# Performance work log

Hardware: AMD Instinct MI355X
Metric: run time of the kernel (lower is better)

The kernel has to match this reference:

```python
import jax, jax.numpy as jnp
import numpy as np

HP, WP = 8, 8          # stoken_size
N_ITER = 2             # refinement iterations
EPS = 1e-12


def unfold3(x):
    """3x3 neighborhood extraction (identity-kernel conv2d, padding=1).
    x: (B, C, hh, ww) -> (B, C, 9, hh, ww); channel k = shift (k//3-1, k%3-1)."""
    B, C, hh, ww = x.shape
    xp = jnp.pad(x, ((0, 0), (0, 0), (1, 1), (1, 1)))
    return jnp.stack([xp[:, :, i:i + hh, j:j + ww]
                      for i in range(3) for j in range(3)], axis=2)


def fold3(x):
    """Transpose of unfold3 (identity-kernel conv_transpose2d, padding=1).
    x: (N, 9, hh, ww) -> (N, hh, ww) via scatter-add of the 9 shifted planes."""
    N, _, hh, ww = x.shape
    out = jnp.zeros((N, hh + 2, ww + 2), x.dtype)
    for idx in range(9):
        i, j = idx // 3, idx % 3
        out = out.at[:, i:i + hh, j:j + ww].add(x[:, idx])
    return out[:, 1:1 + hh, 1:1 + ww]


def _forward(x):
    B, C, H, W = x.shape
    hh, ww = H // HP, W // WP
    M, L = hh * ww, HP * WP
    scale = C ** -0.5

    # initial super-tokens: average pool over each (HP, WP) patch
    xg = x.reshape(B, C, hh, HP, ww, WP)
    stoken = xg.mean(axis=(3, 5))                                  # (B,C,hh,ww)
    pixels = xg.transpose(0, 2, 4, 3, 5, 1).reshape(B, M, L, C)    # (B,M,L,C)

    affinity = None
    for itr in range(N_ITER):
        # 9 neighboring super-tokens per patch: (B,M,C,9)
        st_unf = jnp.transpose(unfold3(stoken), (0, 3, 4, 1, 2)).reshape(B, M, C, 9)
        affinity = jax.nn.softmax(
            jnp.einsum('bmlc,bmcn->bmln', pixels, st_unf) * scale, axis=-1)
        if itr < N_ITER - 1:
            # refine super-tokens: affinity-weighted pixel sums, fold-normalized
            st = jnp.einsum('bmlc,bmln->bmcn', pixels, affinity)   # (B,M,C,9)
            st = fold3(st.transpose(0, 2, 3, 1).reshape(B * C, 9, hh, ww))
            st = st.reshape(B, C, hh, ww)
            norm = fold3(affinity.sum(2).transpose(0, 2, 1).reshape(B, 9, hh, ww)) + EPS
            stoken = st / norm[:, None]

    # broadcast refined super-tokens back to pixels
    st_unf = jnp.transpose(unfold3(stoken), (0, 3, 4, 1, 2)).reshape(B, M, C, 9)
    pix = jnp.einsum('bmcn,bmln->bmcl', st_unf, affinity)          # (B,M,C,L)
    pix = pix.reshape(B, hh, ww, C, HP, WP).transpose(0, 3, 1, 4, 2, 5)
    return pix.reshape(B, C, H, W)


def setup_inputs() -> dict:
    key = jax.random.key(0)
    x = jax.random.normal(key, (4, 384, 224, 224), dtype=jnp.float32)
    return {"x": x}


def reference(x):
    return _forward(x)
```

## Files before the change

kernel.cpp:

```cpp
#include <hip/hip_runtime.h>
#include <cstdint>
#include <cstddef>

typedef __attribute__((ext_vector_type(8))) unsigned short us8;
typedef __attribute__((ext_vector_type(8))) short short8;
typedef __attribute__((ext_vector_type(4))) float f4v;

#define B_ 4
#define C_ 384
#define H_ 224
#define W_ 224
#define HH 28
#define WW 28
#define HW_ (H_*W_)
#define M_ (HH*WW)
#define SCALE_ 0.05103103630798288f
#define EPS_ 1e-12f

__device__ __forceinline__ unsigned short f2bf(float f) {
    union { float f; unsigned int u; } v; v.f = f;
    unsigned int r = v.u + 0x7FFFu + ((v.u >> 16) & 1u);
    return (unsigned short)(r >> 16);
}
__device__ __forceinline__ float bf2f(unsigned short h) {
    union { unsigned int u; float f; } v; v.u = ((unsigned int)h) << 16;
    return v.f;
}

__global__ __launch_bounds__(896) void k_tp(const float* __restrict__ x,
                                            unsigned short* __restrict__ pix,
                                            unsigned short* __restrict__ stokenBF) {
    int bid = blockIdx.x;
    int cg = bid % 12; int t2 = bid / 12; int py = t2 % HH; int b = t2 / HH;
    int tid = threadIdx.x;
    int w = tid >> 2;
    int oct = tid & 3;
    int pxx = w >> 3, qq = w & 7;
    int cbase = cg * 32 + oct * 8;

    const float* xb = x + ((size_t)(b * C_ + cbase) * H_ + py * 8) * W_ + w;
    unsigned short* pb = pix + (((size_t)b * M_ + py * WW + pxx) * 64) * C_ + cbase;

    float v[8][8];
    #pragma unroll
    for (int j = 0; j < 8; ++j)
        #pragma unroll
        for (int pp = 0; pp < 8; ++pp)
            v[pp][j] = xb[(size_t)j * HW_ + (size_t)pp * W_];

    #pragma unroll
    for (int pp = 0; pp < 8; ++pp) {
        us8 o;
        #pragma unroll
        for (int j = 0; j < 8; ++j) o[j] = f2bf(v[pp][j]);
        *(us8*)(pb + (size_t)(pp * 8 + qq) * C_) = o;
    }

    float psum[8];
    #pragma unroll
    for (int j = 0; j < 8; ++j) {
        float s = 0.f;
        #pragma unroll
        for (int pp = 0; pp < 8; ++pp) s += v[pp][j];
        s += __shfl_xor(s, 4);
        s += __shfl_xor(s, 8);
        s += __shfl_xor(s, 16);
        psum[j] = s;
    }
    int lane = tid & 63;
    if ((lane & 28) == 0) {
        us8 o;
        #pragma unroll
        for (int j = 0; j < 8; ++j) o[j] = f2bf(psum[j] * (1.f / 64.f));
        *(us8*)(stokenBF + ((size_t)b * M_ + py * WW + pxx) * C_ + cbase) = o;
    }
}

__device__ __forceinline__ f4v qk_wave(const unsigned short* __restrict__ pixP,
                                       const unsigned short* __restrict__ bfbase,
                                       int b, int py, int pxx, int mt) {
    int lane = threadIdx.x & 63;
    int n = lane & 15, g = lane >> 4;
    int yy = py + n / 3 - 1, xx = pxx + n % 3 - 1;
    bool valid = (n < 9) && yy >= 0 && yy < HH && xx >= 0 && xx < WW;
    size_t cell = valid ? ((size_t)b * M_ + (size_t)yy * WW + xx) : 0;
    const unsigned short* bp = bfbase + cell * C_ + g * 8;
    const unsigned short* ap = pixP + (size_t)(mt * 16 + n) * C_ + g * 8;
    const short8 zz = {0, 0, 0, 0, 0, 0, 0, 0};
    f4v acc = {0.f, 0.f, 0.f, 0.f};
    #pragma unroll
    for (int kt = 0; kt < 12; ++kt) {
        short8 a = *(const short8*)(ap + kt * 32);
        short8 bv = *(const short8*)(bp + kt * 32);
        if (!valid) bv = zz;
        acc = __builtin_amdgcn_mfma_f32_16x16x32_bf16(a, bv, acc, 0, 0, 0);
    }
    return acc;
}

__device__ __forceinline__ void softmax_wave(const f4v s, float aout[4]) {
    int lane = threadIdx.x & 63;
    bool coln = (lane & 15) < 9;
    float v[4], e[4], mx[4], su[4];
    #pragma unroll
    for (int r = 0; r < 4; ++r) v[r] = coln ? s[r] * SCALE_ : -3e38f;
    #pragma unroll
    for (int r = 0; r < 4; ++r) mx[r] = v[r];
    #pragma unroll
    for (int d = 1; d < 16; d <<= 1)
        #pragma unroll
        for (int r = 0; r < 4; ++r) mx[r] = fmaxf(mx[r], __shfl_xor(mx[r], d));
    #pragma unroll
    for (int r = 0; r < 4; ++r) e[r] = coln ? __expf(v[r] - mx[r]) : 0.f;
    #pragma unroll
    for (int r = 0; r < 4; ++r) su[r] = e[r];
    #pragma unroll
    for (int d = 1; d < 16; d <<= 1)
        #pragma unroll
        for (int r = 0; r < 4; ++r) su[r] += __shfl_xor(su[r], d);
    #pragma unroll
    for (int r = 0; r < 4; ++r) aout[r] = e[r] / su[r];
}

__global__ __launch_bounds__(256) void k_it0(const unsigned short* __restrict__ pix,
                                             const unsigned short* __restrict__ stokenBF,
                                             float* __restrict__ st_part,
                                             float* __restrict__ normpart) {
    int bid = blockIdx.x;
    int m = bid % M_, b = bid / M_;
    int py = m / WW, pxx = m - py * WW;
    int tid = threadIdx.x;
    int wid = tid >> 6, lane = tid & 63;
    int n = lane & 15, g = lane >> 4;

    __shared__ float aff32[64][12];
    __shared__ float npart[4][16];

    const unsigned short* pixP = pix + (size_t)bid * 64 * C_;
    f4v s = qk_wave(pixP, stokenBF, b, py, pxx, wid);
    float a[4];
    softmax_wave(s, a);

    if (n < 9) {
        #pragma unroll
        for (int r = 0; r < 4; ++r) aff32[wid * 16 + g * 4 + r][n] = a[r];
    }
    float p = a[0] + a[1] + a[2] + a[3];
    p += __shfl_xor(p, 16);
    p += __shfl_xor(p, 32);
    if (lane < 9) npart[wid][lane] = p;
    __syncthreads();

    if (tid < 9)
        normpart[(size_t)bid * 9 + tid] =
            npart[0][tid] + npart[1][tid] + npart[2][tid] + npart[3][tid];

    for (int c = tid; c < C_; c += 256) {
        float acc9[9];
        #pragma unroll
        for (int k = 0; k < 9; ++k) acc9[k] = 0.f;
        const unsigned short* pb = pixP + c;
        for (int l = 0; l < 64; ++l) {
            float pv = bf2f(pb[(size_t)l * C_]);
            const float4* arow = (const float4*)aff32[l];
            float4 a0 = arow[0], a1 = arow[1];
            float a8 = aff32[l][8];
            acc9[0] += pv * a0.x; acc9[1] += pv * a0.y;
            acc9[2] += pv * a0.z; acc9[3] += pv * a0.w;
            acc9[4] += pv * a1.x; acc9[5] += pv * a1.y;
            acc9[6] += pv * a1.z; acc9[7] += pv * a1.w;
            acc9[8] += pv * a8;
        }
        #pragma unroll
        for (int k = 0; k < 9; ++k)
            st_part[((size_t)bid * 9 + k) * C_ + c] = acc9[k];
    }
}

__global__ __launch_bounds__(256) void k_fold(const float* __restrict__ st_part,
                                              const float* __restrict__ normpart,
                                              float* __restrict__ refined,
                                              unsigned short* __restrict__ refinedBF) {
    int bid = blockIdx.x;
    int cell = bid % M_, b = bid / M_;
    int cy = cell / WW, cx = cell - cy * WW;
    int tid = threadIdx.x;

    float nsum = 0.f;
    int srcm[9]; int nsrc = 0;
    #pragma unroll
    for (int nn = 0; nn < 9; ++nn) {
        int my = cy - (nn / 3 - 1), mx = cx - (nn % 3 - 1);
        if (my >= 0 && my < HH && mx >= 0 && mx < WW) {
            int mm = my * WW + mx;
            srcm[nsrc] = mm * 9 + nn;
            nsum += normpart[(size_t)b * M_ * 9 + mm * 9 + nn];
            ++nsrc;
        }
    }
    float inv = 1.f / (nsum + EPS_);
    for (int c = tid; c < C_; c += 256) {
        float s = 0.f;
        for (int k = 0; k < nsrc; ++k)
            s += st_part[((size_t)b * M_ * 9 + srcm[k]) * C_ + c];
        float r = s * inv;
        refined[((size_t)b * M_ + cell) * C_ + c] = r;
        refinedBF[((size_t)b * M_ + cell) * C_ + c] = f2bf(r);
    }
}

__global__ __launch_bounds__(256) void k_aff(const unsigned short* __restrict__ pix,
                                             const unsigned short* __restrict__ refinedBF,
                                             float* __restrict__ afft) {
    int bid = blockIdx.x;
    int m = bid % M_, b = bid / M_;
    int py = m / WW, pxx = m - py * WW;
    int tid = threadIdx.x;
    int wid = tid >> 6, lane = tid & 63;
    int n = lane & 15, g = lane >> 4;

    const unsigned short* pixP = pix + (size_t)bid * 64 * C_;
    f4v s = qk_wave(pixP, refinedBF, b, py, pxx, wid);
    float a[4];
    softmax_wave(s, a);

    if (n < 9) {
        #pragma unroll
        for (int r = 0; r < 4; ++r) {
            int l = wid * 16 + g * 4 + r;
            int pp = l >> 3, qq = l & 7;
            afft[((((size_t)b * HH + py) * 8 + pp) * 9 + n) * W_ + pxx * 8 + qq] = a[r];
        }
    }
}

__global__ __launch_bounds__(896) void k_out(const float* __restrict__ refined,
                                             const float* __restrict__ afft,
                                             float* __restrict__ out) {
    int bid = blockIdx.x;
    int cg = bid % 12; int t2 = bid / 12; int py = t2 % HH; int b = t2 / HH;
    int c0 = cg * 32;
    int tid = threadIdx.x;
    int w = tid % 224, ci = tid / 224;
    int pxx = w >> 3;

    __shared__ float stub[3][30][33];
    for (int idx = tid; idx < 3 * 30 * 32; idx += 896) {
        int r = idx / 960; int rem = idx - r * 960;
        int xxp = rem >> 5; int cc = rem & 31;
        int yy = py + r - 1, xx = xxp - 1;
        float v = 0.f;
        if (yy >= 0 && yy < HH && xx >= 0 && xx < WW)
            v = refined[((size_t)b * M_ + yy * WW + xx) * C_ + c0 + cc];
        stub[r][xxp][cc] = v;
    }
    __syncthreads();

    const float* ab = afft + (((size_t)b * HH + py) * 8) * 9 * W_ + w;
    float* ob = out + ((size_t)(b * C_) * H_ + py * 8) * W_ + w;

    #pragma unroll
    for (int kh = 0; kh < 2; ++kh) {
        float sreg[9][4];
        #pragma unroll
        for (int nn = 0; nn < 9; ++nn)
            #pragma unroll
            for (int k = 0; k < 4; ++k)
                sreg[nn][k] = stub[nn / 3][pxx + nn % 3][ci + (kh * 4 + k) * 4];
        for (int pp = 0; pp < 8; ++pp) {
            float an[9];
            #pragma unroll
            for (int nn = 0; nn < 9; ++nn)
                an[nn] = ab[(size_t)(pp * 9 + nn) * W_];
            #pragma unroll
            for (int k = 0; k < 4; ++k) {
                float s = 0.f;
                #pragma unroll
                for (int nn = 0; nn < 9; ++nn) s += sreg[nn][k] * an[nn];
                ob[(size_t)(c0 + ci + (kh * 4 + k) * 4) * HW_ + (size_t)pp * W_] = s;
            }
        }
    }
}

__global__ __launch_bounds__(256) void o_pool(const float* __restrict__ x,
                                              float* __restrict__ stoken) {
    int bid = blockIdx.x;
    int yy = bid % HH;
    int t  = bid / HH;
    int c  = t % C_;
    int b  = t / C_;
    __shared__ float colsum[W_];
    int q = threadIdx.x;
    if (q < W_) {
        const float* base = x + ((size_t)(b * C_ + c) * H_ + yy * 8) * W_ + q;
        float s = 0.f;
        #pragma unroll
        for (int p = 0; p < 8; ++p) s += base[(size_t)p * W_];
        colsum[q] = s;
    }
    __syncthreads();
    if (q < WW) {
        float s = 0.f;
        #pragma unroll
        for (int j = 0; j < 8; ++j) s += colsum[q * 8 + j];
        stoken[(((size_t)b * HH + yy) * WW + q) * C_ + c] = s * (1.f / 64.f);
    }
}

__global__ __launch_bounds__(256) void o_iter0(const float* __restrict__ x,
                                               const float* __restrict__ stoken,
                                               float* __restrict__ raw,
                                               float* __restrict__ norm) {
    int bid = blockIdx.x;
    int m = bid % M_;
    int b = bid / M_;
    int py = m / WW, pxx = m % WW;
    int tid = threadIdx.x;
    int w = tid >> 6, l = tid & 63;
    int pp = l >> 3, qq = l & 7;

    __shared__ unsigned short pixs[C_][66];
    __shared__ float sbuf[2304];
    __shared__ float aff[64][10];
    unsigned short* stub = (unsigned short*)sbuf;

    for (int idx = tid; idx < 9 * C_; idx += 256) {
        int nn = idx / C_, c = idx - nn * C_;
        int yy = py + nn / 3 - 1, xx = pxx + nn % 3 - 1;
        float v = 0.f;
        if (yy >= 0 && yy < HH && xx >= 0 && xx < WW)
            v = stoken[(((size_t)b * HH + yy) * WW + xx) * C_ + c];
        stub[idx] = f2bf(v);
    }
    __syncthreads();

    const float* pxbase = x + (size_t)b * C_ * HW_ + (size_t)(py * 8 + pp) * W_ + (pxx * 8 + qq);
    float acc[9];
    #pragma unroll
    for (int nn = 0; nn < 9; ++nn) acc[nn] = 0.f;
    int c0 = w * 96;
    #pragma unroll 4
    for (int c = c0; c < c0 + 96; ++c) {
        float pv = pxbase[(size_t)c * HW_];
        pixs[c][l] = f2bf(pv);
        #pragma unroll
        for (int nn = 0; nn < 9; ++nn) acc[nn] += pv * bf2f(stub[nn * C_ + c]);
    }
    __syncthreads();
    float* qkred = sbuf;
    #pragma unroll
    for (int nn = 0; nn < 9; ++nn) qkred[tid * 9 + nn] = acc[nn];
    __syncthreads();

    if (tid < 64) {
        float s[9];
        #pragma unroll
        for (int nn = 0; nn < 9; ++nn)
            s[nn] = (qkred[(0 * 64 + tid) * 9 + nn] + qkred[(1 * 64 + tid) * 9 + nn] +
                     qkred[(2 * 64 + tid) * 9 + nn] + qkred[(3 * 64 + tid) * 9 + nn]) * SCALE_;
        float mx = s[0];
        #pragma unroll
        for (int nn = 1; nn < 9; ++nn) mx = fmaxf(mx, s[nn]);
        float den = 0.f;
        #pragma unroll
        for (int nn = 0; nn < 9; ++nn) { float e = __expf(s[nn] - mx); den += e; s[nn] = e; }
        float inv = 1.f / den;
        #pragma unroll
        for (int nn = 0; nn < 9; ++nn) aff[tid][nn] = s[nn] * inv;
    }
    __syncthreads();

    if (tid < 9) {
        float s = 0.f;
        for (int ll = 0; ll < 64; ++ll) s += aff[ll][tid];
        int ty = py + tid / 3 - 1, tx = pxx + tid % 3 - 1;
        if (ty >= 0 && ty < HH && tx >= 0 && tx < WW)
            atomicAdd(&norm[((size_t)b * HH + ty) * WW + tx], s);
    }

    for (int c = tid; c < C_; c += 256) {
        float a2[9];
        #pragma unroll
        for (int nn = 0; nn < 9; ++nn) a2[nn] = 0.f;
        for (int ll = 0; ll < 64; ++ll) {
            float pv = bf2f(pixs[c][ll]);
            #pragma unroll
            for (int nn = 0; nn < 9; ++nn) a2[nn] += pv * aff[ll][nn];
        }
        #pragma unroll
        for (int nn = 0; nn < 9; ++nn) {
            int ty = py + nn / 3 - 1, tx = pxx + nn % 3 - 1;
            if (ty >= 0 && ty < HH && tx >= 0 && tx < WW)
                atomicAdd(&raw[(((size_t)b * HH + ty) * WW + tx) * C_ + c], a2[nn]);
        }
    }
}

__global__ __launch_bounds__(256) void o_final(const float* __restrict__ x,
                                               const float* __restrict__ raw,
                                               const float* __restrict__ norm,
                                               float* __restrict__ out) {
    int bid = blockIdx.x;
    int m = bid % M_;
    int b = bid / M_;
    int py = m / WW, pxx = m % WW;
    int tid = threadIdx.x;
    int w = tid >> 6, l = tid & 63;
    int pp = l >> 3, qq = l & 7;

    __shared__ unsigned short stub[9 * C_];
    __shared__ float qkred[4 * 64 * 9];
    __shared__ float aff[64][10];

    for (int idx = tid; idx < 9 * C_; idx += 256) {
        int nn = idx / C_, c = idx - nn * C_;
        int yy = py + nn / 3 - 1, xx = pxx + nn % 3 - 1;
        float v = 0.f;
        if (yy >= 0 && yy < HH && xx >= 0 && xx < WW) {
            size_t cell = ((size_t)b * HH + yy) * WW + xx;
            v = raw[cell * C_ + c] / (norm[cell] + EPS_);
        }
        stub[idx] = f2bf(v);
    }
    __syncthreads();

    const float* pxbase = x + (size_t)b * C_ * HW_ + (size_t)(py * 8 + pp) * W_ + (pxx * 8 + qq);
    float acc[9];
    #pragma unroll
    for (int nn = 0; nn < 9; ++nn) acc[nn] = 0.f;
    int c0 = w * 96;
    #pragma unroll 4
    for (int c = c0; c < c0 + 96; ++c) {
        float pv = pxbase[(size_t)c * HW_];
        #pragma unroll
        for (int nn = 0; nn < 9; ++nn) acc[nn] += pv * bf2f(stub[nn * C_ + c]);
    }
    #pragma unroll
    for (int nn = 0; nn < 9; ++nn) qkred[tid * 9 + nn] = acc[nn];
    __syncthreads();

    if (tid < 64) {
        float s[9];
        #pragma unroll
        for (int nn = 0; nn < 9; ++nn)
            s[nn] = (qkred[(0 * 64 + tid) * 9 + nn] + qkred[(1 * 64 + tid) * 9 + nn] +
                     qkred[(2 * 64 + tid) * 9 + nn] + qkred[(3 * 64 + tid) * 9 + nn]) * SCALE_;
        float mx = s[0];
        #pragma unroll
        for (int nn = 1; nn < 9; ++nn) mx = fmaxf(mx, s[nn]);
        float den = 0.f;
        #pragma unroll
        for (int nn = 0; nn < 9; ++nn) { float e = __expf(s[nn] - mx); den += e; s[nn] = e; }
        float inv = 1.f / den;
        #pragma unroll
        for (int nn = 0; nn < 9; ++nn) aff[tid][nn] = s[nn] * inv;
    }
    __syncthreads();

    float areg[9];
    #pragma unroll
    for (int nn = 0; nn < 9; ++nn) areg[nn] = aff[l][nn];
    float* obase = out + (size_t)b * C_ * HW_ + (size_t)(py * 8 + pp) * W_ + (pxx * 8 + qq);
    #pragma unroll 4
    for (int c = c0; c < c0 + 96; ++c) {
        float v = 0.f;
        #pragma unroll
        for (int nn = 0; nn < 9; ++nn) v += bf2f(stub[nn * C_ + c]) * areg[nn];
        obase[(size_t)c * HW_] = v;
    }
}

extern "C" void kernel_launch(void* const* d_in, const int* in_sizes, int n_in,
                              void* d_out, int out_size, void* d_ws, size_t ws_size,
                              hipStream_t stream) {
    const float* x = (const float*)d_in[0];
    float* out = (float*)d_out;

    const size_t PIXN = (size_t)B_ * M_ * 64 * C_;
    const size_t STN  = (size_t)B_ * M_ * C_;
    const size_t AFFN = (size_t)B_ * HH * 8 * 9 * W_;
    const size_t need = PIXN * 2 + STN * 2 + STN * 2
                      + (STN * 10 + (size_t)B_ * M_ * 9 + AFFN) * 4;

    if (ws_size >= need) {
        unsigned short* pix       = (unsigned short*)d_ws;
        unsigned short* stokenBF  = pix + PIXN;
        unsigned short* refinedBF = stokenBF + STN;
        float* st_part  = (float*)(refinedBF + STN);
        float* refined  = st_part + STN * 9;
        float* normpart = refined + STN;
        float* afft     = normpart + (size_t)B_ * M_ * 9;

        k_tp  <<<B_ * HH * 12, 896, 0, stream>>>(x, pix, stokenBF);
        k_it0 <<<B_ * M_,      256, 0, stream>>>(pix, stokenBF, st_part, normpart);
        k_fold<<<B_ * M_,      256, 0, stream>>>(st_part, normpart, refined, refinedBF);
        k_aff <<<B_ * M_,      256, 0, stream>>>(pix, refinedBF, afft);
        k_out <<<B_ * HH * 12, 896, 0, stream>>>(refined, afft, out);
    } else {
        float* stoken = (float*)d_ws;
        float* raw    = stoken + STN;
        float* norm   = raw + STN;
        hipMemsetAsync(raw, 0, STN * sizeof(float), stream);
        hipMemsetAsync(norm, 0, (size_t)B_ * M_ * sizeof(float), stream);
        o_pool <<<B_ * C_ * HH, 256, 0, stream>>>(x, stoken);
        o_iter0<<<B_ * M_,      256, 0, stream>>>(x, stoken, raw, norm);
        o_final<<<B_ * M_,      256, 0, stream>>>(x, raw, norm, out);
    }
}
```

Before: 340.4 us.

## Restructure k_out to split by width halves and keep affinities in registers

The output kernel's blocks now each cover half an image row of super-tokens across all 384 channels, instead of one 32-channel group over the full width. The 72 affinity values per pixel column are loaded into registers once and reused for every channel, so the 12x re-reading of afft from global memory goes away. Super-token values are read from a padded shared tile with float4 loads. The cost is far fewer blocks (224 vs 1344), a larger shared-memory tile of about 74 KB, and higher register pressure, which may reduce occupancy and latency hiding on the store-heavy output.

```diff
diff --git a/kernel.cpp b/kernel.cpp
--- a/kernel.cpp
+++ b/kernel.cpp
@@ -238,46 +238,51 @@
                                              const float* __restrict__ afft,
                                              float* __restrict__ out) {
     int bid = blockIdx.x;
-    int cg = bid % 12; int t2 = bid / 12; int py = t2 % HH; int b = t2 / HH;
-    int c0 = cg * 32;
-    int tid = threadIdx.x;
-    int w = tid % 224, ci = tid / 224;
+    int half = bid & 1; int t2 = bid >> 1; int py = t2 % HH; int b = t2 / HH;
+    int tid = threadIdx.x;
+    int w = tid % 112, ci = tid / 112;
     int pxx = w >> 3;
 
-    __shared__ float stub[3][30][33];
-    for (int idx = tid; idx < 3 * 30 * 32; idx += 896) {
-        int r = idx / 960; int rem = idx - r * 960;
-        int xxp = rem >> 5; int cc = rem & 31;
-        int yy = py + r - 1, xx = xxp - 1;
+    __shared__ float stub[3 * 16 * 388];
+
+    for (int idx = tid; idx < 3 * 16 * 384; idx += 896) {
+        int ch = idx % 384; int t = idx / 384;
+        int xxp = t % 16; int r = t / 16;
+        int yy = py + r - 1, xx = half * 14 + xxp - 1;
         float v = 0.f;
         if (yy >= 0 && yy < HH && xx >= 0 && xx < WW)
-            v = refined[((size_t)b * M_ + yy * WW + xx) * C_ + c0 + cc];
-        stub[r][xxp][cc] = v;
-    }
-    __syncthreads();
-
-    const float* ab = afft + (((size_t)b * HH + py) * 8) * 9 * W_ + w;
-    float* ob = out + ((size_t)(b * C_) * H_ + py * 8) * W_ + w;
-
-    #pragma unroll
-    for (int kh = 0; kh < 2; ++kh) {
-        float sreg[9][4];
+            v = refined[((size_t)b * M_ + yy * WW + xx) * C_ + ch];
+        stub[(r * 16 + xxp) * 388 + ch] = v;
+    }
+
+    float an[8][9];
+    const float* ab = afft + (((size_t)b * HH + py) * 8) * 9 * W_ + half * 112 + w;
+    #pragma unroll
+    for (int pp = 0; pp < 8; ++pp)
         #pragma unroll
         for (int nn = 0; nn < 9; ++nn)
+            an[pp][nn] = ab[(size_t)(pp * 9 + nn) * W_];
+    __syncthreads();
+
+    float* ob = out + ((size_t)b * C_ * H_ + (size_t)py * 8) * W_ + half * 112 + w;
+
+    for (int kq = 0; kq < 12; ++kq) {
+        int ch = ci * 48 + kq * 4;
+        float sv[9][4];
+        #pragma unroll
+        for (int nn = 0; nn < 9; ++nn) {
+            int r = nn / 3, dx = nn % 3;
+            float4 v4 = *(const float4*)&stub[(r * 16 + pxx + dx) * 388 + ch];
+            sv[nn][0] = v4.x; sv[nn][1] = v4.y; sv[nn][2] = v4.z; sv[nn][3] = v4.w;
+        }
+        #pragma unroll
+        for (int pp = 0; pp < 8; ++pp) {
             #pragma unroll
-            for (int k = 0; k < 4; ++k)
-                sreg[nn][k] = stub[nn / 3][pxx + nn % 3][ci + (kh * 4 + k) * 4];
-        for (int pp = 0; pp < 8; ++pp) {
-            float an[9];
-            #pragma unroll
-            for (int nn = 0; nn < 9; ++nn)
-                an[nn] = ab[(size_t)(pp * 9 + nn) * W_];
-            #pragma unroll
-            for (int k = 0; k < 4; ++k) {
+            for (int j = 0; j < 4; ++j) {
                 float s = 0.f;
                 #pragma unroll
-                for (int nn = 0; nn < 9; ++nn) s += sreg[nn][k] * an[nn];
-                ob[(size_t)(c0 + ci + (kh * 4 + k) * 4) * HW_ + (size_t)pp * W_] = s;
+                for (int nn = 0; nn < 9; ++nn) s += sv[nn][j] * an[pp][nn];
+                ob[((size_t)(ch + j) * H_ + pp) * W_] = s;
             }
         }
     }
@@ -496,7 +501,7 @@
         k_it0 <<<B_ * M_,      256, 0, stream>>>(pix, stokenBF, st_part, normpart);
         k_fold<<<B_ * M_,      256, 0, stream>>>(st_part, normpart, refined, refinedBF);
         k_aff <<<B_ * M_,      256, 0, stream>>>(pix, refinedBF, afft);
-        k_out <<<B_ * HH * 12, 896, 0, stream>>>(refined, afft, out);
+        k_out <<<B_ * HH * 2,  896, 0, stream>>>(refined, afft, out);
     } else {
         float* stoken = (float*)d_ws;
         float* raw    = stoken + STN;
```

Result: slower. 459.4 us (+35.0%).
